# Kernel tuning notes

Hardware: AMD Instinct MI355X
Metric: run time of the kernel (lower is better)

## Reference

```python
import jax, jax.numpy as jnp
import numpy as np


def setup_inputs() -> dict:
    key = jax.random.key(0)
    k1, k2, k3, k4 = jax.random.split(key, 4)
    B, S, IN, OUT = 4, 2048, 4096, 4096
    input = jax.random.normal(k1, (B, S, IN), dtype=jnp.float32)
    int8_weights = jax.random.randint(k2, (OUT, IN), -128, 128, dtype=jnp.int8)
    scales = jax.random.normal(k3, (OUT,), dtype=jnp.float32)
    bias = jax.random.normal(k4, (1, OUT), dtype=jnp.float32)
    return {"input": input, "int8_weights": int8_weights, "scales": scales, "bias": bias}


def reference(input, int8_weights, scales, bias):
    # F.linear(input, W): input @ W.T ; W dequantized by casting to input dtype
    w = int8_weights.astype(input.dtype)              # [OUT, IN] dequant copy
    out = jnp.einsum('bsi,oi->bso', input, w)          # [B, S, OUT]
    out = out * scales                                 # per-output-channel scale
    out = out + bias                                   # broadcast (1, OUT)
    return out
```

## Files before the change

kernel.cpp:

```cpp
#include <hip/hip_runtime.h>
#include <hip/hip_bf16.h>
#include <stdint.h>


typedef __attribute__((ext_vector_type(4))) int i32x4;
typedef __attribute__((ext_vector_type(4))) float f32x4;

__global__ __launch_bounds__(256) void cvt_a_q8(const float* __restrict__ in,
                                                char* __restrict__ outq,
                                                float* __restrict__ ascale,
                                                int K) {
  int row = blockIdx.x * 4 + (threadIdx.x >> 6);
  int lane = threadIdx.x & 63;
  const float4* src = (const float4*)(in + (size_t)row * K);
  const int J = K >> 8;
  float amax = 0.f;
#pragma unroll 4
  for (int j = 0; j < J; ++j) {
    float4 v = src[j * 64 + lane];
    amax = fmaxf(amax, fmaxf(fmaxf(fabsf(v.x), fabsf(v.y)),
                             fmaxf(fabsf(v.z), fabsf(v.w))));
  }
#pragma unroll
  for (int s = 32; s; s >>= 1) amax = fmaxf(amax, __shfl_xor(amax, s));
  float scale = amax > 0.f ? amax / 127.f : 1.f;
  float inv = amax > 0.f ? 127.f / amax : 0.f;
  if (lane == 0) ascale[row] = scale;
  int* dst = (int*)(outq + (size_t)row * K);
#pragma unroll 4
  for (int j = 0; j < J; ++j) {
    float4 v = src[j * 64 + lane];
    int a = __float2int_rn(v.x * inv) & 255;
    int b = __float2int_rn(v.y * inv) & 255;
    int c = __float2int_rn(v.z * inv) & 255;
    int d = __float2int_rn(v.w * inv) & 255;
    dst[j * 64 + lane] = a | (b << 8) | (c << 16) | (d << 24);
  }
}

__global__ __launch_bounds__(256) void cvt_w_q8(const int* __restrict__ in,
                                                char* __restrict__ out) {
  long i = (long)blockIdx.x * 256 + threadIdx.x;
  const int4* p = (const int4*)in + 4 * i;
  int4 a = p[0], b = p[1], c = p[2], d = p[3];
  uint4 r;
  r.x = (a.x & 255) | ((a.y & 255) << 8) | ((a.z & 255) << 16) | ((unsigned)(a.w & 255) << 24);
  r.y = (b.x & 255) | ((b.y & 255) << 8) | ((b.z & 255) << 16) | ((unsigned)(b.w & 255) << 24);
  r.z = (c.x & 255) | ((c.y & 255) << 8) | ((c.z & 255) << 16) | ((unsigned)(c.w & 255) << 24);
  r.w = (d.x & 255) | ((d.y & 255) << 8) | ((d.z & 255) << 16) | ((unsigned)(d.w & 255) << 24);
  ((uint4*)out)[i] = r;
}

__device__ __forceinline__ void gl_lds16(const void* g, void* l) {
  __builtin_amdgcn_global_load_lds(
      (const __attribute__((address_space(1))) void*)g,
      (__attribute__((address_space(3))) void*)l,
      16, 0, 0);
}

__device__ __forceinline__ void stage2c(const char* src, size_t rows8,
                                        char* dst) {
  gl_lds16(src, dst);
  gl_lds16(src + rows8, dst + 1024);
}

#define WAIT_LGKM(N) do { asm volatile("s_waitcnt lgkmcnt(" #N ")" ::: "memory"); \
                          __builtin_amdgcn_sched_barrier(0); } while (0)
#define WAIT_VM(N)   asm volatile("s_waitcnt vmcnt(" #N ")" ::: "memory")
#define BAR()        do { asm volatile("" ::: "memory"); \
                          __builtin_amdgcn_s_barrier(); \
                          asm volatile("" ::: "memory"); } while (0)
#define SBAR0()      __builtin_amdgcn_sched_barrier(0)

#define BM 256
#define BN 256
#define BKT 128

template <int MI0>
__device__ __forceinline__ void mfma_quad(i32x4 (&acc)[8][4],
                                          const i32x4 (&a)[2][2],
                                          const i32x4 (&b)[4][2]) {
  __builtin_amdgcn_s_setprio(1);
#pragma unroll
  for (int m = 0; m < 2; ++m)
#pragma unroll
    for (int ni = 0; ni < 4; ++ni)
#pragma unroll
      for (int kk = 0; kk < 2; ++kk)
        acc[MI0 + m][ni] = __builtin_amdgcn_mfma_i32_16x16x64_i8(
            a[m][kk], b[ni][kk], acc[MI0 + m][ni], 0, 0, 0);
  __builtin_amdgcn_s_setprio(0);
}

#define RD_AQ(dst, Pq, MI0)                                                  \
  do {                                                                       \
    dst[0][0] = *(const i32x4*)(ldsB + offA[Pq][0] + (MI0) * 2048);          \
    dst[0][1] = *(const i32x4*)(ldsB + offA[Pq][1] + (MI0) * 2048);          \
    dst[1][0] = *(const i32x4*)(ldsB + offA[Pq][0] + (MI0 + 1) * 2048);      \
    dst[1][1] = *(const i32x4*)(ldsB + offA[Pq][1] + (MI0 + 1) * 2048);      \
  } while (0)

#define RD_B(dst, Pq)                                                        \
  do {                                                                       \
    _Pragma("unroll")                                                        \
    for (int ni = 0; ni < 4; ++ni) {                                         \
      dst[ni][0] = *(const i32x4*)(ldsB + offB[Pq][0] + ni * 2048);          \
      dst[ni][1] = *(const i32x4*)(ldsB + offB[Pq][1] + ni * 2048);          \
    }                                                                        \
  } while (0)

#define ST_A(U, H, PB)                                                       \
  stage2c(gA_st + (size_t)(H) * 128 * Kb + (size_t)(U) * BKT, Kb8,           \
          ldsB + (PB) * 65536 + (H) * 16384 + stOffB)
#define ST_B(U, H, PB)                                                       \
  stage2c(gB_st + (size_t)(H) * 128 * Kb + (size_t)(U) * BKT, Kb8,           \
          ldsB + (PB) * 65536 + 32768 + (H) * 16384 + stOffB)

#define KT(U, P)                                                              \
  do {                                                                        \
    const int u_ = (U);                                                       \
                                                                      \
    RD_AQ(aY, P, 2);                                                          \
    if (u_ + 1 < NT) ST_A(u_ + 1, 1, (P) ^ 1);                                \
    WAIT_LGKM(4);                             \
    BAR();                                                        \
    mfma_quad<0>(acc, aX, bfr);                                               \
                                                                      \
    RD_AQ(aX, P, 4);                                                          \
    if (u_ + 2 < NT) ST_B(u_ + 2, 0, P);                                      \
    WAIT_LGKM(4);                                      \
    mfma_quad<2>(acc, aY, bfr);                                               \
                                                                      \
    RD_AQ(aY, P, 6);                                                          \
    if (u_ + 2 < NT) ST_B(u_ + 2, 1, P);                                      \
    WAIT_LGKM(4);                                      \
    mfma_quad<4>(acc, aX, bfr);                                               \
    WAIT_LGKM(0);               \
                                                                      \
    if (u_ + 2 < NT)      { WAIT_VM(4); }                                     \
    else if (u_ + 1 < NT) { WAIT_VM(0); }                                     \
    BAR();                       \
    if (u_ + 2 < NT) ST_A(u_ + 2, 0, P);                                      \
    if (u_ + 1 < NT) RD_AQ(aX, (P) ^ 1, 0);                                   \
    SBAR0();                                                                  \
    mfma_quad<6>(acc, aY, bfr);                                               \
    SBAR0();                \
    if (u_ + 1 < NT) RD_B(bfr, (P) ^ 1);                                      \
  } while (0)

__global__ __launch_bounds__(512, 2) void gemm8_kernel(
    const char* __restrict__ Aq,
    const char* __restrict__ Wq,
    const float* __restrict__ ascale,
    const float* __restrict__ scales,
    const float* __restrict__ bias,
    float* __restrict__ out,
    int M, int N, int K) {
  __shared__ char lds[2][65536];
  char* ldsB = &lds[0][0];

  const int tid = threadIdx.x;
  const int lane = tid & 63;
  const int w = tid >> 6;
  const int wr = w >> 2;
  const int wc = w & 3;
  const int r = lane & 15;
  const int q4 = lane >> 4;
  const int NT = K / BKT;
  const size_t Kb = (size_t)K;
  const size_t Kb8 = 8 * Kb;

  const int nm = M / BM, nn_t = N / BN;
  const int nwg = gridDim.x;
  const int bid = blockIdx.x;
  int tile_m, tile_n;
  if (nm == 32 && nn_t == 16 && nwg == 512) {
    int xcd = bid & 7;
    int j = bid >> 3;
    tile_m = (j >> 4) * 8 + xcd;
    tile_n = j & 15;
  } else {
    int swz = bid;
    if ((nwg & 7) == 0) swz = (bid & 7) * (nwg >> 3) + (bid >> 3);
    tile_m = swz % nm;
    tile_n = swz / nm;
  }
  const int bm = tile_m * BM;
  const int bn = tile_n * BN;

  const int lk0 = r * 128 + ((q4 ^ (r & 3)) << 4) + ((((r >> 2) & 1)) << 6);
  const int lk1 = r * 128 + ((q4 ^ (r & 3)) << 4) + ((1 ^ ((r >> 2) & 1)) << 6);
  int offA[2][2], offB[2][2];
#pragma unroll
  for (int p = 0; p < 2; ++p) {
    offA[p][0] = p * 65536 + wr * 16384 + lk0;
    offA[p][1] = p * 65536 + wr * 16384 + lk1;
    offB[p][0] = p * 65536 + 32768 + (wc >> 1) * 16384 + (wc & 1) * 8192 + lk0;
    offB[p][1] = p * 65536 + 32768 + (wc >> 1) * 16384 + (wc & 1) * 8192 + lk1;
  }

  const int rl = lane >> 3;
  const int gs = (lane & 7) ^ (rl & 7);
  const int stOffB = w * 2048 + lane * 16;
  const char* gA_st = Aq + ((size_t)bm + w * 16 + rl) * Kb + gs * 16;
  const char* gB_st = Wq + ((size_t)bn + w * 16 + rl) * Kb + gs * 16;

  ST_A(0, 0, 0);
  ST_A(0, 1, 0);
  ST_B(0, 0, 0);
  ST_B(0, 1, 0);
  ST_B(1, 0, 1);
  ST_B(1, 1, 1);
  ST_A(1, 0, 1);
  WAIT_VM(6);
  BAR();

  i32x4 acc[8][4] = {};
  i32x4 bfr[4][2];
  i32x4 aX[2][2], aY[2][2];

  RD_AQ(aX, 0, 0);
  RD_B(bfr, 0);

  for (int t = 0; t < NT; t += 2) {
    KT(t, 0);
    KT(t + 1, 1);
  }

  float sc[4], bs[4];
#pragma unroll
  for (int ni = 0; ni < 4; ++ni) {
    int col = bn + wc * 64 + ni * 16 + r;
    sc[ni] = scales[col];
    bs[ni] = bias[col];
  }
#pragma unroll
  for (int mi = 0; mi < 8; ++mi) {
    float as_[4];
#pragma unroll
    for (int i = 0; i < 4; ++i)
      as_[i] = ascale[bm + wr * 128 + mi * 16 + q4 * 4 + i];
#pragma unroll
    for (int ni = 0; ni < 4; ++ni)
#pragma unroll
      for (int i = 0; i < 4; ++i) {
        int grow = bm + wr * 128 + mi * 16 + q4 * 4 + i;
        int gcol = bn + wc * 64 + ni * 16 + r;
        out[(size_t)grow * N + gcol] =
            (float)acc[mi][ni][i] * (as_[i] * sc[ni]) + bs[ni];
      }
  }
}

__global__ __launch_bounds__(256) void naive_kernel(
    const float* __restrict__ A, const int* __restrict__ W8,
    const float* __restrict__ scales, const float* __restrict__ bias,
    float* __restrict__ out, int M, int N, int K) {
  long idx = (long)blockIdx.x * 256 + threadIdx.x;
  if (idx >= (long)M * N) return;
  int m = (int)(idx / N), n = (int)(idx % N);
  const float* a = A + (size_t)m * K;
  const int* wv = W8 + (size_t)n * K;
  float s = 0.f;
  for (int k = 0; k < K; ++k) s += a[k] * (float)wv[k];
  out[idx] = s * scales[n] + bias[n];
}

extern "C" void kernel_launch(void* const* d_in, const int* in_sizes, int n_in,
                              void* d_out, int out_size, void* d_ws, size_t ws_size,
                              hipStream_t stream) {
  const float* A = (const float*)d_in[0];
  const int* W8 = (const int*)d_in[1];
  const float* scales = (const float*)d_in[2];
  const float* bias = (const float*)d_in[3];
  float* out = (float*)d_out;

  const int N = in_sizes[2];
  const int K = in_sizes[1] / N;
  const int M = in_sizes[0] / K;

  size_t aq_bytes = (size_t)M * K;
  size_t as_bytes = (size_t)M * 4;
  size_t wq_bytes = (size_t)N * K;
  const int NT = K / BKT;

  bool tiled_ok = (M % BM == 0) && (N % BN == 0) && (K % BKT == 0) &&
                  (K % 256 == 0) && (K <= 4096) && (M % 4 == 0) &&
                  ((long)N * K % 4096 == 0) &&
                  (NT >= 4) && (NT % 2 == 0) &&
                  (ws_size >= aq_bytes + as_bytes + wq_bytes);

  if (!tiled_ok) {
    long total = (long)M * N;
    naive_kernel<<<(unsigned)((total + 255) / 256), 256, 0, stream>>>(
        A, W8, scales, bias, out, M, N, K);
    return;
  }

  char* Aq = (char*)d_ws;
  float* ascale = (float*)((char*)d_ws + aq_bytes);
  char* Wq = (char*)d_ws + aq_bytes + as_bytes;

  cvt_a_q8<<<(unsigned)(M / 4), 256, 0, stream>>>(A, Aq, ascale, K);
  long nW = (long)N * K;
  cvt_w_q8<<<(unsigned)(nW / 4096), 256, 0, stream>>>(W8, Wq);

  unsigned nwg = (unsigned)((M / BM) * (N / BN));
  gemm8_kernel<<<nwg, 512, 0, stream>>>(Aq, Wq, ascale, scales, bias, out,
                                        M, N, K);
}
```

Measured before the change: 197.7 us.

## Shrink GEMM tiles to 128x128 with 256 threads and merge quantize prep kernels

Changes the int8 GEMM block tile from 256x256 with 8 waves to 128x128 with 4 waves, halving LDS per buffer and rewriting the staging, fragment reads and tile swizzle to match. Also fuses the activation-quantize and weight-pack kernels into one launch. The goal is more workgroups and better occupancy, and one fewer launch. In exchange, smaller tiles lower arithmetic intensity and raise global/L2 traffic for A and B.

After: 200.3 us. Within noise of the previous version (+1.3%).

```diff
diff --git a/kernel.cpp b/kernel.cpp
--- a/kernel.cpp
+++ b/kernel.cpp
@@ -4,51 +4,52 @@
 
 
 typedef __attribute__((ext_vector_type(4))) int i32x4;
-typedef __attribute__((ext_vector_type(4))) float f32x4;
-
-__global__ __launch_bounds__(256) void cvt_a_q8(const float* __restrict__ in,
-                                                char* __restrict__ outq,
-                                                float* __restrict__ ascale,
-                                                int K) {
-  int row = blockIdx.x * 4 + (threadIdx.x >> 6);
-  int lane = threadIdx.x & 63;
-  const float4* src = (const float4*)(in + (size_t)row * K);
-  const int J = K >> 8;
-  float amax = 0.f;
+
+__global__ __launch_bounds__(256) void prep_q8(const float* __restrict__ A,
+                                               const int* __restrict__ W8,
+                                               char* __restrict__ Aq,
+                                               float* __restrict__ ascale,
+                                               char* __restrict__ Wq,
+                                               int K, int nblkA) {
+  int bid = blockIdx.x;
+  if (bid < nblkA) {
+    int row = bid * 4 + (threadIdx.x >> 6);
+    int lane = threadIdx.x & 63;
+    const float4* src = (const float4*)(A + (size_t)row * K);
+    const int J = K >> 8;
+    float amax = 0.f;
 #pragma unroll 4
-  for (int j = 0; j < J; ++j) {
-    float4 v = src[j * 64 + lane];
-    amax = fmaxf(amax, fmaxf(fmaxf(fabsf(v.x), fabsf(v.y)),
-                             fmaxf(fabsf(v.z), fabsf(v.w))));
-  }
-#pragma unroll
-  for (int s = 32; s; s >>= 1) amax = fmaxf(amax, __shfl_xor(amax, s));
-  float scale = amax > 0.f ? amax / 127.f : 1.f;
-  float inv = amax > 0.f ? 127.f / amax : 0.f;
-  if (lane == 0) ascale[row] = scale;
-  int* dst = (int*)(outq + (size_t)row * K);
+    for (int j = 0; j < J; ++j) {
+      float4 v = src[j * 64 + lane];
+      amax = fmaxf(amax, fmaxf(fmaxf(fabsf(v.x), fabsf(v.y)),
+                               fmaxf(fabsf(v.z), fabsf(v.w))));
+    }
+#pragma unroll
+    for (int s = 32; s; s >>= 1) amax = fmaxf(amax, __shfl_xor(amax, s));
+    float scale = amax > 0.f ? amax / 127.f : 1.f;
+    float inv = amax > 0.f ? 127.f / amax : 0.f;
+    if (lane == 0) ascale[row] = scale;
+    int* dst = (int*)(Aq + (size_t)row * K);
 #pragma unroll 4
-  for (int j = 0; j < J; ++j) {
-    float4 v = src[j * 64 + lane];
-    int a = __float2int_rn(v.x * inv) & 255;
-    int b = __float2int_rn(v.y * inv) & 255;
-    int c = __float2int_rn(v.z * inv) & 255;
-    int d = __float2int_rn(v.w * inv) & 255;
-    dst[j * 64 + lane] = a | (b << 8) | (c << 16) | (d << 24);
-  }
-}
-
-__global__ __launch_bounds__(256) void cvt_w_q8(const int* __restrict__ in,
-                                                char* __restrict__ out) {
-  long i = (long)blockIdx.x * 256 + threadIdx.x;
-  const int4* p = (const int4*)in + 4 * i;
-  int4 a = p[0], b = p[1], c = p[2], d = p[3];
-  uint4 r;
-  r.x = (a.x & 255) | ((a.y & 255) << 8) | ((a.z & 255) << 16) | ((unsigned)(a.w & 255) << 24);
-  r.y = (b.x & 255) | ((b.y & 255) << 8) | ((b.z & 255) << 16) | ((unsigned)(b.w & 255) << 24);
-  r.z = (c.x & 255) | ((c.y & 255) << 8) | ((c.z & 255) << 16) | ((unsigned)(c.w & 255) << 24);
-  r.w = (d.x & 255) | ((d.y & 255) << 8) | ((d.z & 255) << 16) | ((unsigned)(d.w & 255) << 24);
-  ((uint4*)out)[i] = r;
+    for (int j = 0; j < J; ++j) {
+      float4 v = src[j * 64 + lane];
+      int a = __float2int_rn(v.x * inv) & 255;
+      int b = __float2int_rn(v.y * inv) & 255;
+      int c = __float2int_rn(v.z * inv) & 255;
+      int d = __float2int_rn(v.w * inv) & 255;
+      dst[j * 64 + lane] = a | (b << 8) | (c << 16) | (d << 24);
+    }
+  } else {
+    long i = (long)(bid - nblkA) * 256 + threadIdx.x;
+    const int4* p = (const int4*)W8 + 4 * i;
+    int4 a = p[0], b = p[1], c = p[2], d = p[3];
+    uint4 r;
+    r.x = (a.x & 255) | ((a.y & 255) << 8) | ((a.z & 255) << 16) | ((unsigned)(a.w & 255) << 24);
+    r.y = (b.x & 255) | ((b.y & 255) << 8) | ((b.z & 255) << 16) | ((unsigned)(b.w & 255) << 24);
+    r.z = (c.x & 255) | ((c.y & 255) << 8) | ((c.z & 255) << 16) | ((unsigned)(c.w & 255) << 24);
+    r.w = (d.x & 255) | ((d.y & 255) << 8) | ((d.z & 255) << 16) | ((unsigned)(d.w & 255) << 24);
+    ((uint4*)Wq)[i] = r;
+  }
 }
 
 __device__ __forceinline__ void gl_lds16(const void* g, void* l) {
@@ -56,12 +57,6 @@
       (const __attribute__((address_space(1))) void*)g,
       (__attribute__((address_space(3))) void*)l,
       16, 0, 0);
-}
-
-__device__ __forceinline__ void stage2c(const char* src, size_t rows8,
-                                        char* dst) {
-  gl_lds16(src, dst);
-  gl_lds16(src + rows8, dst + 1024);
 }
 
 #define WAIT_LGKM(N) do { asm volatile("s_waitcnt lgkmcnt(" #N ")" ::: "memory"); \
@@ -72,32 +67,28 @@
                           asm volatile("" ::: "memory"); } while (0)
 #define SBAR0()      __builtin_amdgcn_sched_barrier(0)
 
-#define BM 256
-#define BN 256
+#define BM 128
+#define BN 128
 #define BKT 128
 
-template <int MI0>
-__device__ __forceinline__ void mfma_quad(i32x4 (&acc)[8][4],
-                                          const i32x4 (&a)[2][2],
-                                          const i32x4 (&b)[4][2]) {
+template <int MI>
+__device__ __forceinline__ void mfma_m(i32x4 (&acc)[4][4],
+                                       const i32x4 (&a)[2],
+                                       const i32x4 (&b)[4][2]) {
   __builtin_amdgcn_s_setprio(1);
 #pragma unroll
-  for (int m = 0; m < 2; ++m)
-#pragma unroll
-    for (int ni = 0; ni < 4; ++ni)
-#pragma unroll
-      for (int kk = 0; kk < 2; ++kk)
-        acc[MI0 + m][ni] = __builtin_amdgcn_mfma_i32_16x16x64_i8(
-            a[m][kk], b[ni][kk], acc[MI0 + m][ni], 0, 0, 0);
+  for (int ni = 0; ni < 4; ++ni)
+#pragma unroll
+    for (int kk = 0; kk < 2; ++kk)
+      acc[MI][ni] = __builtin_amdgcn_mfma_i32_16x16x64_i8(
+          a[kk], b[ni][kk], acc[MI][ni], 0, 0, 0);
   __builtin_amdgcn_s_setprio(0);
 }
 
-#define RD_AQ(dst, Pq, MI0)                                                  \
+#define RD_A2(dst, Pq, MI)                                                   \
   do {                                                                       \
-    dst[0][0] = *(const i32x4*)(ldsB + offA[Pq][0] + (MI0) * 2048);          \
-    dst[0][1] = *(const i32x4*)(ldsB + offA[Pq][1] + (MI0) * 2048);          \
-    dst[1][0] = *(const i32x4*)(ldsB + offA[Pq][0] + (MI0 + 1) * 2048);      \
-    dst[1][1] = *(const i32x4*)(ldsB + offA[Pq][1] + (MI0 + 1) * 2048);      \
+    dst[0] = *(const i32x4*)(ldsB + offA[Pq][0] + (MI) * 2048);              \
+    dst[1] = *(const i32x4*)(ldsB + offA[Pq][1] + (MI) * 2048);              \
   } while (0)
 
 #define RD_B(dst, Pq)                                                        \
@@ -110,45 +101,53 @@
   } while (0)
 
 #define ST_A(U, H, PB)                                                       \
-  stage2c(gA_st + (size_t)(H) * 128 * Kb + (size_t)(U) * BKT, Kb8,           \
-          ldsB + (PB) * 65536 + (H) * 16384 + stOffB)
+  do {                                                                       \
+    const char* s_ = gA_st + (size_t)(H) * 64 * Kb + (size_t)(U) * BKT;      \
+    char* d_ = ldsB + (PB) * 32768 + (H) * 8192 + stLds;                     \
+    gl_lds16(s_, d_);                                                        \
+    gl_lds16(s_ + Kb32, d_ + 4096);                                          \
+  } while (0)
 #define ST_B(U, H, PB)                                                       \
-  stage2c(gB_st + (size_t)(H) * 128 * Kb + (size_t)(U) * BKT, Kb8,           \
-          ldsB + (PB) * 65536 + 32768 + (H) * 16384 + stOffB)
+  do {                                                                       \
+    const char* s_ = gB_st + (size_t)(H) * 64 * Kb + (size_t)(U) * BKT;      \
+    char* d_ = ldsB + (PB) * 32768 + 16384 + (H) * 8192 + stLds;             \
+    gl_lds16(s_, d_);                                                        \
+    gl_lds16(s_ + Kb32, d_ + 4096);                                          \
+  } while (0)
 
 #define KT(U, P)                                                              \
   do {                                                                        \
     const int u_ = (U);                                                       \
                                                                       \
-    RD_AQ(aY, P, 2);                                                          \
+    RD_A2(aY, P, 1);                                                          \
     if (u_ + 1 < NT) ST_A(u_ + 1, 1, (P) ^ 1);                                \
-    WAIT_LGKM(4);                             \
+    WAIT_LGKM(2);                                                             \
     BAR();                                                        \
-    mfma_quad<0>(acc, aX, bfr);                                               \
+    mfma_m<0>(acc, aX, bfr);                                                  \
                                                                       \
-    RD_AQ(aX, P, 4);                                                          \
+    RD_A2(aX, P, 2);                                                          \
     if (u_ + 2 < NT) ST_B(u_ + 2, 0, P);                                      \
-    WAIT_LGKM(4);                                      \
-    mfma_quad<2>(acc, aY, bfr);                                               \
+    WAIT_LGKM(2);                                                             \
+    mfma_m<1>(acc, aY, bfr);                                                  \
                                                                       \
-    RD_AQ(aY, P, 6);                                                          \
+    RD_A2(aY, P, 3);                                                          \
     if (u_ + 2 < NT) ST_B(u_ + 2, 1, P);                                      \
-    WAIT_LGKM(4);                                      \
-    mfma_quad<4>(acc, aX, bfr);                                               \
-    WAIT_LGKM(0);               \
+    WAIT_LGKM(2);                                                             \
+    mfma_m<2>(acc, aX, bfr);                                                  \
+    WAIT_LGKM(0);                                                             \
                                                                       \
     if (u_ + 2 < NT)      { WAIT_VM(4); }                                     \
     else if (u_ + 1 < NT) { WAIT_VM(0); }                                     \
-    BAR();                       \
+    BAR();                                                        \
     if (u_ + 2 < NT) ST_A(u_ + 2, 0, P);                                      \
-    if (u_ + 1 < NT) RD_AQ(aX, (P) ^ 1, 0);                                   \
+    if (u_ + 1 < NT) RD_A2(aX, (P) ^ 1, 0);                                   \
     SBAR0();                                                                  \
-    mfma_quad<6>(acc, aY, bfr);                                               \
-    SBAR0();                \
+    mfma_m<3>(acc, aY, bfr);                                                  \
+    SBAR0();            \
     if (u_ + 1 < NT) RD_B(bfr, (P) ^ 1);                                      \
   } while (0)
 
-__global__ __launch_bounds__(512, 2) void gemm8_kernel(
+__global__ __launch_bounds__(256, 2) void gemm8_kernel(
     const char* __restrict__ Aq,
     const char* __restrict__ Wq,
     const float* __restrict__ ascale,
@@ -156,29 +155,31 @@
     const float* __restrict__ bias,
     float* __restrict__ out,
     int M, int N, int K) {
-  __shared__ char lds[2][65536];
+  __shared__ char lds[2][32768];
   char* ldsB = &lds[0][0];
 
   const int tid = threadIdx.x;
   const int lane = tid & 63;
   const int w = tid >> 6;
-  const int wr = w >> 2;
-  const int wc = w & 3;
+  const int wr = w >> 1;
+  const int wc = w & 1;
   const int r = lane & 15;
   const int q4 = lane >> 4;
   const int NT = K / BKT;
   const size_t Kb = (size_t)K;
-  const size_t Kb8 = 8 * Kb;
+  const size_t Kb32 = 32 * Kb;
 
   const int nm = M / BM, nn_t = N / BN;
   const int nwg = gridDim.x;
   const int bid = blockIdx.x;
   int tile_m, tile_n;
-  if (nm == 32 && nn_t == 16 && nwg == 512) {
+  if (nm == 64 && nn_t == 32 && nwg == 2048) {
     int xcd = bid & 7;
     int j = bid >> 3;
-    tile_m = (j >> 4) * 8 + xcd;
-    tile_n = j & 15;
+    int s = j & 63;
+    int g = j >> 6;
+    tile_m = (s & 7) * 8 + xcd;
+    tile_n = g * 8 + (s >> 3);
   } else {
     int swz = bid;
     if ((nwg & 7) == 0) swz = (bid & 7) * (nwg >> 3) + (bid >> 3);
@@ -193,17 +194,16 @@
   int offA[2][2], offB[2][2];
 #pragma unroll
   for (int p = 0; p < 2; ++p) {
-    offA[p][0] = p * 65536 + wr * 16384 + lk0;
-    offA[p][1] = p * 65536 + wr * 16384 + lk1;
-    offB[p][0] = p * 65536 + 32768 + (wc >> 1) * 16384 + (wc & 1) * 8192 + lk0;
-    offB[p][1] = p * 65536 + 32768 + (wc >> 1) * 16384 + (wc & 1) * 8192 + lk1;
-  }
-
-  const int rl = lane >> 3;
-  const int gs = (lane & 7) ^ (rl & 7);
-  const int stOffB = w * 2048 + lane * 16;
-  const char* gA_st = Aq + ((size_t)bm + w * 16 + rl) * Kb + gs * 16;
-  const char* gB_st = Wq + ((size_t)bn + w * 16 + rl) * Kb + gs * 16;
+    offA[p][0] = p * 32768 + wr * 8192 + lk0;
+    offA[p][1] = p * 32768 + wr * 8192 + lk1;
+    offB[p][0] = p * 32768 + 16384 + wc * 8192 + lk0;
+    offB[p][1] = p * 32768 + 16384 + wc * 8192 + lk1;
+  }
+
+  const int gs = (tid & 7) ^ ((tid >> 3) & 7);
+  const int stLds = tid * 16;
+  const char* gA_st = Aq + ((size_t)bm + (tid >> 3)) * Kb + gs * 16;
+  const char* gB_st = Wq + ((size_t)bn + (tid >> 3)) * Kb + gs * 16;
 
   ST_A(0, 0, 0);
   ST_A(0, 1, 0);
@@ -215,11 +215,11 @@
   WAIT_VM(6);
   BAR();
 
-  i32x4 acc[8][4] = {};
+  i32x4 acc[4][4] = {};
   i32x4 bfr[4][2];
-  i32x4 aX[2][2], aY[2][2];
-
-  RD_AQ(aX, 0, 0);
+  i32x4 aX[2], aY[2];
+
+  RD_A2(aX, 0, 0);
   RD_B(bfr, 0);
 
   for (int t = 0; t < NT; t += 2) {
@@ -235,16 +235,16 @@
     bs[ni] = bias[col];
   }
 #pragma unroll
-  for (int mi = 0; mi < 8; ++mi) {
+  for (int mi = 0; mi < 4; ++mi) {
     float as_[4];
 #pragma unroll
     for (int i = 0; i < 4; ++i)
-      as_[i] = ascale[bm + wr * 128 + mi * 16 + q4 * 4 + i];
+      as_[i] = ascale[bm + wr * 64 + mi * 16 + q4 * 4 + i];
 #pragma unroll
     for (int ni = 0; ni < 4; ++ni)
 #pragma unroll
       for (int i = 0; i < 4; ++i) {
-        int grow = bm + wr * 128 + mi * 16 + q4 * 4 + i;
+        int grow = bm + wr * 64 + mi * 16 + q4 * 4 + i;
         int gcol = bn + wc * 64 + ni * 16 + r;
         out[(size_t)grow * N + gcol] =
             (float)acc[mi][ni][i] * (as_[i] * sc[ni]) + bs[ni];
@@ -285,7 +285,7 @@
   const int NT = K / BKT;
 
   bool tiled_ok = (M % BM == 0) && (N % BN == 0) && (K % BKT == 0) &&
-                  (K % 256 == 0) && (K <= 4096) && (M % 4 == 0) &&
+                  (K % 256 == 0) && (M % 4 == 0) &&
                   ((long)N * K % 4096 == 0) &&
                   (NT >= 4) && (NT % 2 == 0) &&
                   (ws_size >= aq_bytes + as_bytes + wq_bytes);
@@ -301,11 +301,12 @@
   float* ascale = (float*)((char*)d_ws + aq_bytes);
   char* Wq = (char*)d_ws + aq_bytes + as_bytes;
 
-  cvt_a_q8<<<(unsigned)(M / 4), 256, 0, stream>>>(A, Aq, ascale, K);
+  int nblkA = M / 4;
   long nW = (long)N * K;
-  cvt_w_q8<<<(unsigned)(nW / 4096), 256, 0, stream>>>(W8, Wq);
+  unsigned nblkW = (unsigned)(nW / 4096);
+  prep_q8<<<nblkA + nblkW, 256, 0, stream>>>(A, W8, Aq, ascale, Wq, K, nblkA);
 
   unsigned nwg = (unsigned)((M / BM) * (N / BN));
-  gemm8_kernel<<<nwg, 512, 0, stream>>>(Aq, Wq, ascale, scales, bias, out,
+  gemm8_kernel<<<nwg, 256, 0, stream>>>(Aq, Wq, ascale, scales, bias, out,
                                         M, N, K);
 }
```
